# Kernel tuning notes

Hardware: AMD Instinct MI355X
Metric: run time of the kernel (lower is better)

## Reference

```python
import jax, jax.numpy as jnp
import numpy as np

B, S, H = 16, 2048, 1024

def setup_inputs() -> dict:
    key = jax.random.key(0)
    ks = jax.random.split(key, 6)
    return {
        "h": jax.random.normal(ks[0], (1, B, H), jnp.float32),
        "c": jax.random.normal(ks[1], (1, B, H), jnp.float32),
        "encoder_outputs": jax.random.normal(ks[2], (B, S, H), jnp.float32),
        "attn_W": jax.random.normal(ks[3], (H, 2 * H), jnp.float32) * 0.02,
        "attn_b": jax.random.normal(ks[4], (H,), jnp.float32) * 0.02,
        "v_W": jax.random.normal(ks[5], (1, H), jnp.float32) * 0.02,
    }

def reference(h, c, encoder_outputs, attn_W, attn_b, v_W):
    # h: (1,B,H) -> (B,1,H); a: (B,S,H)
    a = encoder_outputs
    hq = jnp.transpose(h, (1, 0, 2))  # (B,1,H)
    # cat((s, a), -1) @ attn_W.T == s @ Wh.T + a @ Wa.T (avoids (B,S,2H) buffer)
    Wh, Wa = attn_W[:, :H], attn_W[:, H:]
    energy = jax.nn.relu(
        jnp.einsum("bqh,oh->bqo", hq, Wh)          # (B,1,H), broadcast over S
        + jnp.einsum("bsh,oh->bso", a, Wa)
        + attn_b
    )  # (B,S,H)
    scores = jnp.einsum("bsh,h->bs", energy, v_W[0])  # (B,S)
    attn_weights = jax.nn.softmax(scores, axis=1)      # (B,S)
    context = jnp.einsum("bs,bsh->bh", attn_weights, a)[:, None, :]  # (B,1,H)
    return context, attn_weights
```

## Files before the change

### kernel.cpp

```cpp
#include <hip/hip_runtime.h>
#include <hip/hip_bf16.h>


typedef __bf16 bf16x8 __attribute__((ext_vector_type(8)));
typedef float floatx4 __attribute__((ext_vector_type(4)));

#define BB 16
#define SS 2048
#define HH 1024
#define MM (BB * SS)

#define GLB(p) ((const __attribute__((address_space(1))) void*)(p))
#define LDSP(p) ((__attribute__((address_space(3))) void*)(p))

__device__ inline ushort f2bf(float x) {
    uint32_t u = __builtin_bit_cast(uint32_t, x);
    u += 0x7FFFu + ((u >> 16) & 1u);
    return (ushort)(u >> 16);
}

__global__ __launch_bounds__(256) void prep_all_kernel(
    const float* __restrict__ h, const float* __restrict__ W,
    const float* __restrict__ bias, const float* __restrict__ a,
    float* __restrict__ projh, __bf16* __restrict__ Wb, __bf16* __restrict__ Ab,
    float* __restrict__ scores, float* __restrict__ ctx)
{
    int bid = blockIdx.x;
    int tid = threadIdx.x;
    if (bid >= 336) {
        size_t i = (size_t)(bid - 336) * 256 + tid;
        const float* s = a + i * 8;
        float4 x = *(const float4*)(s);
        float4 y = *(const float4*)(s + 4);
        union { ushort u[8]; uint4 v; } p;
        p.u[0] = f2bf(x.x); p.u[1] = f2bf(x.y); p.u[2] = f2bf(x.z); p.u[3] = f2bf(x.w);
        p.u[4] = f2bf(y.x); p.u[5] = f2bf(y.y); p.u[6] = f2bf(y.z); p.u[7] = f2bf(y.w);
        *(uint4*)(Ab + i * 8) = p.v;
    } else if (bid < 256) {
        int b = bid >> 4;
        int oc = bid & 15;
        __shared__ float hrow[HH];
        *(float4*)&hrow[tid * 4] = *(const float4*)(h + (size_t)b * HH + tid * 4);
        __syncthreads();
        int ol = tid >> 2;
        int kq = tid & 3;
        int o = oc * 64 + ol;
        const float* wr = W + (size_t)o * (2 * HH) + kq * 256;
        const float* hb = hrow + kq * 256;
        float sum = 0.f;
        for (int k = 0; k < 256; k += 4) {
            float4 wv = *(const float4*)(wr + k);
            sum += hb[k] * wv.x + hb[k + 1] * wv.y + hb[k + 2] * wv.z + hb[k + 3] * wv.w;
        }
        sum += __shfl_xor(sum, 1);
        sum += __shfl_xor(sum, 2);
        if (kq == 0) projh[b * HH + o] = sum + bias[o];
    } else if (bid < 320) {
        int cb = bid - 256;
#pragma unroll
        for (int j = 0; j < 8; j++) {
            int g = cb * 2048 + tid + j * 256;
            int o = g >> 7;
            int k = (g & 127) * 8;
            const float* s = W + (size_t)o * (2 * HH) + HH + k;
            float4 x = *(const float4*)(s);
            float4 y = *(const float4*)(s + 4);
            union { ushort u[8]; uint4 v; } p;
            p.u[0] = f2bf(x.x); p.u[1] = f2bf(x.y); p.u[2] = f2bf(x.z); p.u[3] = f2bf(x.w);
            p.u[4] = f2bf(y.x); p.u[5] = f2bf(y.y); p.u[6] = f2bf(y.z); p.u[7] = f2bf(y.w);
            *(uint4*)(Wb + (size_t)o * HH + k) = p.v;
        }
    } else {
        int zb = bid - 320;
        float4 z = make_float4(0.f, 0.f, 0.f, 0.f);
        float* sp = scores + zb * 2048 + tid * 8;
        *(float4*)(sp) = z;
        *(float4*)(sp + 4) = z;
        *(float4*)(ctx + zb * 1024 + tid * 4) = z;
    }
}

__global__ __launch_bounds__(512, 2) void gemm_scores_kernel(
    const __bf16* __restrict__ Ab,
    const __bf16* __restrict__ Wb,
    const float* __restrict__ projh,
    const float* __restrict__ vW,
    float* __restrict__ scores)
{
    __shared__ __bf16 smem[32768];

    const int bid = blockIdx.x;
    const int m0 = (((bid >> 5) << 3) + (bid & 7)) * 256;
    const int n0 = ((bid >> 3) & 3) * 256;
    const int bidx = m0 >> 11;

    const int tid = threadIdx.x;
    const int lane = tid & 63;
    const int wave = tid >> 6;
    const int wm = (wave & 1) * 128;
    const int wn = (wave >> 1) * 64;
    const int quad = lane >> 4;
    const int l16 = lane & 15;

    floatx4 acc[8][4];
    const floatx4 z = {0.f, 0.f, 0.f, 0.f};
#pragma unroll
    for (int i = 0; i < 8; i++)
#pragma unroll
        for (int j = 0; j < 4; j++) acc[i][j] = z;

    const int su = tid >> 3;
    const int sj = (tid & 7) ^ (su & 7);
    const int g_row = su * 2 + (sj >> 2);
    const int g_col = (sj & 3) * 8;
    const __bf16* gA  = Ab + (size_t)(m0 + g_row) * HH + g_col;
    const __bf16* gA2 = gA + (size_t)128 * HH;
    const __bf16* gB  = Wb + (size_t)(n0 + g_row) * HH + g_col;
    const __bf16* gB2 = gB + (size_t)128 * HH;
    const int ldsb = wave * 512;

    int aoff[8], boff[4];
#pragma unroll
    for (int i = 0; i < 8; i++) {
        int frow = wm + i * 16 + l16;
        int u2 = frow >> 1;
        int cc = u2 * 8 + (((((frow & 1) << 2) | quad)) ^ (u2 & 7));
        aoff[i] = cc * 8;
    }
#pragma unroll
    for (int j = 0; j < 4; j++) {
        int frow = wn + j * 16 + l16;
        int u2 = frow >> 1;
        int cc = u2 * 8 + (((((frow & 1) << 2) | quad)) ^ (u2 & 7));
        boff[j] = 8192 + cc * 8;
    }

#define ISSUE_STAGE(buf, k0)                                                          \
    {                                                                                 \
        __bf16* dst = smem + (buf) * 16384 + ldsb;                                    \
        __builtin_amdgcn_global_load_lds(GLB(gA  + (k0)), LDSP(dst),         16, 0, 0); \
        __builtin_amdgcn_global_load_lds(GLB(gA2 + (k0)), LDSP(dst + 4096),  16, 0, 0); \
        __builtin_amdgcn_global_load_lds(GLB(gB  + (k0)), LDSP(dst + 8192),  16, 0, 0); \
        __builtin_amdgcn_global_load_lds(GLB(gB2 + (k0)), LDSP(dst + 12288), 16, 0, 0); \
    }

    ISSUE_STAGE(0, 0)
    for (int s = 0; s < 32; s++) {
        __syncthreads();
        if (s < 31) ISSUE_STAGE((s + 1) & 1, (s + 1) * 32)
        const __bf16* sb = smem + (s & 1) * 16384;
        bf16x8 af[8], bfr[4];
#pragma unroll
        for (int j = 0; j < 4; j++) bfr[j] = *(const bf16x8*)(sb + boff[j]);
#pragma unroll
        for (int i = 0; i < 8; i++) af[i] = *(const bf16x8*)(sb + aoff[i]);
#pragma unroll
        for (int i = 0; i < 8; i++)
#pragma unroll
            for (int j = 0; j < 4; j++)
                acc[i][j] = __builtin_amdgcn_mfma_f32_16x16x32_bf16(af[i], bfr[j], acc[i][j], 0, 0, 0);
    }
#undef ISSUE_STAGE

    float ph[4], vv[4];
#pragma unroll
    for (int j = 0; j < 4; j++) {
        int ng = n0 + wn + j * 16 + l16;
        ph[j] = projh[bidx * HH + ng];
        vv[j] = vW[ng];
    }
#pragma unroll
    for (int i = 0; i < 8; i++) {
        float s[4] = {0.f, 0.f, 0.f, 0.f};
#pragma unroll
        for (int j = 0; j < 4; j++) {
#pragma unroll
            for (int r2 = 0; r2 < 4; r2++) {
                float e = acc[i][j][r2] + ph[j];
                e = e > 0.f ? e : 0.f;
                s[r2] += e * vv[j];
            }
        }
#pragma unroll
        for (int r2 = 0; r2 < 4; r2++) {
            s[r2] += __shfl_xor(s[r2], 1);
            s[r2] += __shfl_xor(s[r2], 2);
            s[r2] += __shfl_xor(s[r2], 4);
            s[r2] += __shfl_xor(s[r2], 8);
        }
        if (l16 == 0) {
#pragma unroll
            for (int r2 = 0; r2 < 4; r2++) {
                int mg = m0 + wm + i * 16 + quad * 4 + r2;
                atomicAdd(&scores[mg], s[r2]);
            }
        }
    }
}

__global__ __launch_bounds__(256) void gemm_scores_f32_kernel(
    const float* __restrict__ A, const float* __restrict__ W,
    const float* __restrict__ projh, const float* __restrict__ vW,
    float* __restrict__ scores)
{
    constexpr int BM = 128, BN = 128, BK = 32, LDT = BK + 8;
    __shared__ __bf16 As[BM * LDT];
    __shared__ __bf16 Bs[BN * LDT];
    const int n0 = blockIdx.x * BN;
    const int m0 = blockIdx.y * BM;
    const int bidx = m0 >> 11;
    const int tid = threadIdx.x;
    const int lane = tid & 63;
    const int wave = tid >> 6;
    const int wm = (wave & 1) * 64;
    const int wn = (wave >> 1) * 64;
    const int quad = lane >> 4;
    const int l16 = lane & 15;
    floatx4 acc[4][4];
    const floatx4 z = {0.f, 0.f, 0.f, 0.f};
#pragma unroll
    for (int i = 0; i < 4; i++)
#pragma unroll
        for (int j = 0; j < 4; j++) acc[i][j] = z;
    int rowT[4], colT[4];
#pragma unroll
    for (int i = 0; i < 4; i++) {
        int fi = tid + 256 * i;
        rowT[i] = fi >> 3;
        colT[i] = (fi & 7) * 4;
    }
    for (int k0 = 0; k0 < HH; k0 += BK) {
        float4 av[4], bv[4];
#pragma unroll
        for (int i = 0; i < 4; i++) {
            av[i] = *(const float4*)(A + (size_t)(m0 + rowT[i]) * HH + k0 + colT[i]);
            bv[i] = *(const float4*)(W + (size_t)(n0 + rowT[i]) * (2 * HH) + HH + k0 + colT[i]);
        }
        __syncthreads();
#pragma unroll
        for (int i = 0; i < 4; i++) {
            ushort4 ua = make_ushort4(f2bf(av[i].x), f2bf(av[i].y), f2bf(av[i].z), f2bf(av[i].w));
            ushort4 ub = make_ushort4(f2bf(bv[i].x), f2bf(bv[i].y), f2bf(bv[i].z), f2bf(bv[i].w));
            *(ushort4*)&As[rowT[i] * LDT + colT[i]] = ua;
            *(ushort4*)&Bs[rowT[i] * LDT + colT[i]] = ub;
        }
        __syncthreads();
        bf16x8 af[4], bf[4];
#pragma unroll
        for (int i = 0; i < 4; i++)
            af[i] = *(const bf16x8*)&As[(wm + i * 16 + l16) * LDT + quad * 8];
#pragma unroll
        for (int j = 0; j < 4; j++)
            bf[j] = *(const bf16x8*)&Bs[(wn + j * 16 + l16) * LDT + quad * 8];
#pragma unroll
        for (int i = 0; i < 4; i++)
#pragma unroll
            for (int j = 0; j < 4; j++)
                acc[i][j] = __builtin_amdgcn_mfma_f32_16x16x32_bf16(af[i], bf[j], acc[i][j], 0, 0, 0);
    }
    float ph[4], vv[4];
#pragma unroll
    for (int j = 0; j < 4; j++) {
        int ng = n0 + wn + j * 16 + l16;
        ph[j] = projh[bidx * HH + ng];
        vv[j] = vW[ng];
    }
#pragma unroll
    for (int i = 0; i < 4; i++) {
        float s[4] = {0.f, 0.f, 0.f, 0.f};
#pragma unroll
        for (int j = 0; j < 4; j++) {
#pragma unroll
            for (int r = 0; r < 4; r++) {
                float e = acc[i][j][r] + ph[j];
                e = e > 0.f ? e : 0.f;
                s[r] += e * vv[j];
            }
        }
#pragma unroll
        for (int r = 0; r < 4; r++) {
            s[r] += __shfl_xor(s[r], 1);
            s[r] += __shfl_xor(s[r], 2);
            s[r] += __shfl_xor(s[r], 4);
            s[r] += __shfl_xor(s[r], 8);
        }
        if (l16 == 0) {
#pragma unroll
            for (int r = 0; r < 4; r++) {
                int mg = m0 + wm + i * 16 + quad * 4 + r;
                atomicAdd(&scores[mg], s[r]);
            }
        }
    }
}

__global__ __launch_bounds__(256) void softmax_context_kernel(
    const float* __restrict__ A, const float* __restrict__ scores,
    float* __restrict__ wout, float* __restrict__ ctx)
{
    int b = blockIdx.x >> 5;
    int sc = blockIdx.x & 31;
    int tid = threadIdx.x;
    const float* srow = scores + b * SS;

    float x[8];
    float mx = -1e30f;
#pragma unroll
    for (int i = 0; i < 8; i++) { x[i] = srow[tid + i * 256]; mx = fmaxf(mx, x[i]); }
#pragma unroll
    for (int off = 32; off; off >>= 1) mx = fmaxf(mx, __shfl_xor(mx, off));
    __shared__ float redm[4], reds[4];
    if ((tid & 63) == 0) redm[tid >> 6] = mx;
    __syncthreads();
    mx = fmaxf(fmaxf(redm[0], redm[1]), fmaxf(redm[2], redm[3]));
    float sum = 0.f;
#pragma unroll
    for (int i = 0; i < 8; i++) sum += __expf(x[i] - mx);
#pragma unroll
    for (int off = 32; off; off >>= 1) sum += __shfl_xor(sum, off);
    if ((tid & 63) == 0) reds[tid >> 6] = sum;
    __syncthreads();
    float inv = 1.0f / (reds[0] + reds[1] + reds[2] + reds[3]);

    __shared__ float wsm[64];
    if (tid < 64) {
        float wv = __expf(srow[sc * 64 + tid] - mx) * inv;
        wsm[tid] = wv;
        wout[b * SS + sc * 64 + tid] = wv;
    }
    __syncthreads();

    const float* arow = A + ((size_t)b * SS + sc * 64) * HH + tid * 4;
    float4 acc = make_float4(0.f, 0.f, 0.f, 0.f);
#pragma unroll 4
    for (int s = 0; s < 64; s++) {
        float w = wsm[s];
        float4 v = *(const float4*)(arow + (size_t)s * HH);
        acc.x += w * v.x; acc.y += w * v.y; acc.z += w * v.z; acc.w += w * v.w;
    }
    float* o = ctx + b * HH + tid * 4;
    atomicAdd(o + 0, acc.x);
    atomicAdd(o + 1, acc.y);
    atomicAdd(o + 2, acc.z);
    atomicAdd(o + 3, acc.w);
}

extern "C" void kernel_launch(void* const* d_in, const int* in_sizes, int n_in,
                              void* d_out, int out_size, void* d_ws, size_t ws_size,
                              hipStream_t stream) {
    const float* h    = (const float*)d_in[0];
    const float* a    = (const float*)d_in[2];
    const float* W    = (const float*)d_in[3];
    const float* bias = (const float*)d_in[4];
    const float* vW   = (const float*)d_in[5];
    float* out = (float*)d_out;

    float* projh  = (float*)d_ws;
    float* scores = projh + BB * HH;
    __bf16* Wb = (__bf16*)(scores + MM);
    __bf16* Ab = Wb + (size_t)HH * HH;
    const size_t need = (size_t)(BB * HH + MM) * 4 + (size_t)HH * HH * 2
                      + (size_t)MM * HH * 2;

    if (ws_size >= need) {
        prep_all_kernel<<<336 + MM * HH / 8 / 256, 256, 0, stream>>>(
            h, W, bias, a, projh, Wb, Ab, scores, out);
        gemm_scores_kernel<<<512, 512, 0, stream>>>(Ab, Wb, projh, vW, scores);
    } else {
        prep_all_kernel<<<336, 256, 0, stream>>>(h, W, bias, a, projh, Wb, Ab, scores, out);
        gemm_scores_f32_kernel<<<dim3(HH / 128, MM / 128), 256, 0, stream>>>(a, W, projh, vW, scores);
    }

    softmax_context_kernel<<<BB * 32, 256, 0, stream>>>(a, scores, out + BB * HH, out);
}
```

Before: 295.0 us.

## Reduce scores in LDS per N-quarter and read bf16 encoder copy in context

The GEMM epilogue now accumulates per-row score partials in shared memory and writes one partial per N-quarter to a 4-way partial buffer, replacing global atomics on scores. The softmax/context kernel sums the four partials and reads the bf16 copy of the encoder outputs instead of the fp32 original, halving the bytes read for the context pass. This trades global atomic contention for an extra LDS reduction and sync, and lowers context precision to bf16 inputs. The prep zeroing of scores is now mostly redundant on the fast path.

```diff
diff --git a/kernel.cpp b/kernel.cpp
--- a/kernel.cpp
+++ b/kernel.cpp
@@ -23,7 +23,7 @@
     const float* __restrict__ h, const float* __restrict__ W,
     const float* __restrict__ bias, const float* __restrict__ a,
     float* __restrict__ projh, __bf16* __restrict__ Wb, __bf16* __restrict__ Ab,
-    float* __restrict__ scores, float* __restrict__ ctx)
+    float* __restrict__ sp0, float* __restrict__ ctx)
 {
     int bid = blockIdx.x;
     int tid = threadIdx.x;
@@ -73,7 +73,7 @@
     } else {
         int zb = bid - 320;
         float4 z = make_float4(0.f, 0.f, 0.f, 0.f);
-        float* sp = scores + zb * 2048 + tid * 8;
+        float* sp = sp0 + zb * 2048 + tid * 8;
         *(float4*)(sp) = z;
         *(float4*)(sp + 4) = z;
         *(float4*)(ctx + zb * 1024 + tid * 4) = z;
@@ -85,13 +85,14 @@
     const __bf16* __restrict__ Wb,
     const float* __restrict__ projh,
     const float* __restrict__ vW,
-    float* __restrict__ scores)
+    float* __restrict__ scores_part)
 {
     __shared__ __bf16 smem[32768];
 
     const int bid = blockIdx.x;
     const int m0 = (((bid >> 5) << 3) + (bid & 7)) * 256;
-    const int n0 = ((bid >> 3) & 3) * 256;
+    const int nq = (bid >> 3) & 3;
+    const int n0 = nq * 256;
     const int bidx = m0 >> 11;
 
     const int tid = threadIdx.x;
@@ -169,6 +170,11 @@
         ph[j] = projh[bidx * HH + ng];
         vv[j] = vW[ng];
     }
+
+    float* red = (float*)smem;
+    if (tid < 256) red[tid] = 0.f;
+    __syncthreads();
+
 #pragma unroll
     for (int i = 0; i < 8; i++) {
         float s[4] = {0.f, 0.f, 0.f, 0.f};
@@ -190,12 +196,12 @@
         }
         if (l16 == 0) {
 #pragma unroll
-            for (int r2 = 0; r2 < 4; r2++) {
-                int mg = m0 + wm + i * 16 + quad * 4 + r2;
-                atomicAdd(&scores[mg], s[r2]);
-            }
-        }
-    }
+            for (int r2 = 0; r2 < 4; r2++)
+                atomicAdd(&red[wm + i * 16 + quad * 4 + r2], s[r2]);
+        }
+    }
+    __syncthreads();
+    if (tid < 256) scores_part[(size_t)nq * MM + m0 + tid] = red[tid];
 }
 
 __global__ __launch_bounds__(256) void gemm_scores_f32_kernel(
@@ -295,14 +301,76 @@
 }
 
 __global__ __launch_bounds__(256) void softmax_context_kernel(
-    const float* __restrict__ A, const float* __restrict__ scores,
+    const __bf16* __restrict__ Ab, const float* __restrict__ scores_part,
+    int nparts, float* __restrict__ wout, float* __restrict__ ctx)
+{
+    int b = blockIdx.x >> 5;
+    int sc = blockIdx.x & 31;
+    int tid = threadIdx.x;
+    const float* srow = scores_part + b * SS;
+
+    float x[8];
+    float mx = -1e30f;
+#pragma unroll
+    for (int i = 0; i < 8; i++) {
+        int idx = tid + i * 256;
+        float v = srow[idx];
+        for (int q = 1; q < nparts; q++) v += srow[(size_t)q * MM + idx];
+        x[i] = v; mx = fmaxf(mx, v);
+    }
+#pragma unroll
+    for (int off = 32; off; off >>= 1) mx = fmaxf(mx, __shfl_xor(mx, off));
+    __shared__ float redm[4], reds[4];
+    if ((tid & 63) == 0) redm[tid >> 6] = mx;
+    __syncthreads();
+    mx = fmaxf(fmaxf(redm[0], redm[1]), fmaxf(redm[2], redm[3]));
+    float sum = 0.f;
+#pragma unroll
+    for (int i = 0; i < 8; i++) sum += __expf(x[i] - mx);
+#pragma unroll
+    for (int off = 32; off; off >>= 1) sum += __shfl_xor(sum, off);
+    if ((tid & 63) == 0) reds[tid >> 6] = sum;
+    __syncthreads();
+    float inv = 1.0f / (reds[0] + reds[1] + reds[2] + reds[3]);
+
+    __shared__ float wsm[64];
+    if (tid < 64) {
+        int idx = sc * 64 + tid;
+        float v = srow[idx];
+        for (int q = 1; q < nparts; q++) v += srow[(size_t)q * MM + idx];
+        float wv = __expf(v - mx) * inv;
+        wsm[tid] = wv;
+        wout[b * SS + idx] = wv;
+    }
+    __syncthreads();
+
+    const __bf16* arow = Ab + ((size_t)b * SS + sc * 64) * HH + tid * 4;
+    float4 acc = make_float4(0.f, 0.f, 0.f, 0.f);
+#pragma unroll 4
+    for (int s = 0; s < 64; s++) {
+        float w = wsm[s];
+        uint2 uv = *(const uint2*)(arow + (size_t)s * HH);
+        float a0 = __builtin_bit_cast(float, uv.x << 16);
+        float a1 = __builtin_bit_cast(float, uv.x & 0xffff0000u);
+        float a2 = __builtin_bit_cast(float, uv.y << 16);
+        float a3 = __builtin_bit_cast(float, uv.y & 0xffff0000u);
+        acc.x += w * a0; acc.y += w * a1; acc.z += w * a2; acc.w += w * a3;
+    }
+    float* o = ctx + b * HH + tid * 4;
+    atomicAdd(o + 0, acc.x);
+    atomicAdd(o + 1, acc.y);
+    atomicAdd(o + 2, acc.z);
+    atomicAdd(o + 3, acc.w);
+}
+
+__global__ __launch_bounds__(256) void softmax_context_f32_kernel(
+    const float* __restrict__ A, const float* __restrict__ scores_part,
     float* __restrict__ wout, float* __restrict__ ctx)
 {
     int b = blockIdx.x >> 5;
     int sc = blockIdx.x & 31;
     int tid = threadIdx.x;
-    const float* srow = scores + b * SS;
-
+    const float* srow = scores_part + b * SS;
     float x[8];
     float mx = -1e30f;
 #pragma unroll
@@ -321,7 +389,6 @@
     if ((tid & 63) == 0) reds[tid >> 6] = sum;
     __syncthreads();
     float inv = 1.0f / (reds[0] + reds[1] + reds[2] + reds[3]);
-
     __shared__ float wsm[64];
     if (tid < 64) {
         float wv = __expf(srow[sc * 64 + tid] - mx) * inv;
@@ -329,7 +396,6 @@
         wout[b * SS + sc * 64 + tid] = wv;
     }
     __syncthreads();
-
     const float* arow = A + ((size_t)b * SS + sc * 64) * HH + tid * 4;
     float4 acc = make_float4(0.f, 0.f, 0.f, 0.f);
 #pragma unroll 4
@@ -355,21 +421,24 @@
     const float* vW   = (const float*)d_in[5];
     float* out = (float*)d_out;
 
-    float* projh  = (float*)d_ws;
-    float* scores = projh + BB * HH;
-    __bf16* Wb = (__bf16*)(scores + MM);
+    float* projh       = (float*)d_ws;
+    float* scores_part = projh + BB * HH;
+    __bf16* Wb = (__bf16*)(scores_part + 4 * MM);
     __bf16* Ab = Wb + (size_t)HH * HH;
-    const size_t need = (size_t)(BB * HH + MM) * 4 + (size_t)HH * HH * 2
+    const size_t need = (size_t)(BB * HH + 4 * MM) * 4 + (size_t)HH * HH * 2
                       + (size_t)MM * HH * 2;
 
     if (ws_size >= need) {
         prep_all_kernel<<<336 + MM * HH / 8 / 256, 256, 0, stream>>>(
-            h, W, bias, a, projh, Wb, Ab, scores, out);
-        gemm_scores_kernel<<<512, 512, 0, stream>>>(Ab, Wb, projh, vW, scores);
+            h, W, bias, a, projh, Wb, Ab, scores_part, out);
+        gemm_scores_kernel<<<512, 512, 0, stream>>>(Ab, Wb, projh, vW, scores_part);
+        softmax_context_kernel<<<BB * 32, 256, 0, stream>>>(
+            Ab, scores_part, 4, out + BB * HH, out);
     } else {
-        prep_all_kernel<<<336, 256, 0, stream>>>(h, W, bias, a, projh, Wb, Ab, scores, out);
-        gemm_scores_f32_kernel<<<dim3(HH / 128, MM / 128), 256, 0, stream>>>(a, W, projh, vW, scores);
-    }
-
-    softmax_context_kernel<<<BB * 32, 256, 0, stream>>>(a, scores, out + BB * HH, out);
-}
+        prep_all_kernel<<<336, 256, 0, stream>>>(h, W, bias, a, projh, Wb, Ab, scores_part, out);
+        gemm_scores_f32_kernel<<<dim3(HH / 128, MM / 128), 256, 0, stream>>>(
+            a, W, projh, vW, scores_part);
+        softmax_context_f32_kernel<<<BB * 32, 256, 0, stream>>>(
+            a, scores_part, out + BB * HH, out);
+    }
+}
```

Result: no change. 294.8 us (-0.1%).
